# Performance work log

Measured on AMD Instinct MI355X. Metric: run time of the kernel, lower is better.

The kernel has to match this reference:

```python
import jax, jax.numpy as jnp
import numpy as np

B, M, N = 32, 2048, 2048
W_PRIMAL, W_DUAL, W_STAT, W_COMP = 0.1, 0.1, 0.6, 0.2


def setup_inputs() -> dict:
    key = jax.random.key(0)
    k1, k2, k3, k4, k5 = jax.random.split(key, 5)
    return {
        "x_hat": jax.random.normal(k1, (B * N,), dtype=jnp.float32),
        "lam_hat": jax.random.normal(k2, (B * M,), dtype=jnp.float32),
        "A": jax.random.normal(k3, (B, M, N), dtype=jnp.float32),
        "b_pad": jax.random.normal(k4, (B, M), dtype=jnp.float32),
        "c_pad": jax.random.normal(k5, (B, N), dtype=jnp.float32),
        "b_mask": jnp.ones((B, M), dtype=bool),
        "c_mask": jnp.ones((B, N), dtype=bool),
    }


def reference(x_hat, lam_hat, A, b_pad, c_pad, b_mask, c_mask):
    # Uniform sizes: x_hat is the concatenation of B vectors of length N,
    # lam_hat of B vectors of length M. b_mask/c_mask are unused by the
    # original forward (full padding assumed here).
    b, m, n = A.shape
    x = x_hat.reshape(b, n)
    lam = lam_hat.reshape(b, m)

    # Batched mat-vec products (the spmm calls in the original, fp32 math).
    Ax_minus_b = jnp.einsum("bmn,bn->bm", A, x) - b_pad        # [B, M]
    At_lambda = jnp.einsum("bmn,bm->bn", A, lam)               # [B, N]

    # Per-sample mean, summed over batch, then * (1/B) == global mean
    # (sizes are uniform).
    loss_primal = jnp.mean(jnp.square(jax.nn.relu(Ax_minus_b)))
    loss_dual = jnp.mean(jnp.square(jax.nn.relu(-lam)))
    loss_stat = jnp.mean(jnp.square(At_lambda + c_pad))
    loss_comp = jnp.mean(jnp.square(lam * Ax_minus_b))

    total = (W_PRIMAL * loss_primal + W_DUAL * loss_dual
             + W_STAT * loss_stat + W_COMP * loss_comp)
    return total
```

## Files before the change

### kernel.cpp

```cpp
#include <hip/hip_runtime.h>

#define BB 32
#define MM 2048
#define NN 2048
#define ROWS 64
#define THREADS 256


__device__ __forceinline__ float waveReduceSum(float v) {
#pragma unroll
    for (int off = 32; off > 0; off >>= 1)
        v += __shfl_down(v, off, 64);
    return v;
}

__global__ __launch_bounds__(256) void zero_ws_kernel(float* __restrict__ ws, int n) {
    int i = blockIdx.x * blockDim.x + threadIdx.x;
    if (i < n) ws[i] = 0.0f;
}

__global__ __launch_bounds__(THREADS) void fused_main(
    const float* __restrict__ x_hat, const float* __restrict__ lam_hat,
    const float* __restrict__ A, const float* __restrict__ b_pad,
    float* __restrict__ At, float* __restrict__ acc) {
    const int b = blockIdx.y;
    const int m0 = blockIdx.x * ROWS;
    const int t = threadIdx.x;
    const int wave = t >> 6;
    const int lane = t & 63;

    __shared__ float lamS[ROWS];
    __shared__ float wp[ROWS * 4];

    if (t < ROWS) lamS[t] = lam_hat[b * MM + m0 + t];
    __syncthreads();

    const float4* xv = (const float4*)(x_hat + (size_t)b * NN);
    const float4 x0 = xv[t];
    const float4 x1 = xv[256 + t];

    float4 at0 = make_float4(0.f, 0.f, 0.f, 0.f);
    float4 at1 = make_float4(0.f, 0.f, 0.f, 0.f);

    const float4* Ab = (const float4*)(A + ((size_t)b * MM + (size_t)m0) * NN);

    for (int r = 0; r < ROWS; ++r) {
        const float4* ap = Ab + (size_t)r * (NN / 4);
        float4 a0 = ap[t];
        float4 a1 = ap[256 + t];
        float lm = lamS[r];
        float dot = a0.x * x0.x + a0.y * x0.y + a0.z * x0.z + a0.w * x0.w
                  + a1.x * x1.x + a1.y * x1.y + a1.z * x1.z + a1.w * x1.w;
        at0.x += a0.x * lm; at0.y += a0.y * lm; at0.z += a0.z * lm; at0.w += a0.w * lm;
        at1.x += a1.x * lm; at1.y += a1.y * lm; at1.z += a1.z * lm; at1.w += a1.w * lm;
        float wsum = waveReduceSum(dot);
        if (lane == 0) wp[r * 4 + wave] = wsum;
    }
    __syncthreads();

    if (t < ROWS) {
        int r = t;
        float y = wp[r * 4 + 0] + wp[r * 4 + 1] + wp[r * 4 + 2] + wp[r * 4 + 3]
                - b_pad[b * MM + m0 + r];
        float lm = lamS[r];
        float ry = fmaxf(y, 0.f);
        float pr = ry * ry;
        float cm = lm * y;
        cm = cm * cm;
        pr = waveReduceSum(pr);
        cm = waveReduceSum(cm);
        if (t == 0) {
            atomicAdd(&acc[0], pr);
            atomicAdd(&acc[1], cm);
        }
    }

    float* Atb = At + (size_t)b * NN;
    int c0 = t * 4;
    atomicAdd(&Atb[c0 + 0], at0.x);
    atomicAdd(&Atb[c0 + 1], at0.y);
    atomicAdd(&Atb[c0 + 2], at0.z);
    atomicAdd(&Atb[c0 + 3], at0.w);
    atomicAdd(&Atb[1024 + c0 + 0], at1.x);
    atomicAdd(&Atb[1024 + c0 + 1], at1.y);
    atomicAdd(&Atb[1024 + c0 + 2], at1.z);
    atomicAdd(&Atb[1024 + c0 + 3], at1.w);
}

__global__ __launch_bounds__(256) void finalize_partial(
    const float* __restrict__ At, const float* __restrict__ c_pad,
    const float* __restrict__ lam_hat, float* __restrict__ acc) {
    int idx = blockIdx.x * blockDim.x + threadIdx.x;
    int stride = gridDim.x * blockDim.x;
    float stat = 0.f, dual = 0.f;
    for (int i = idx; i < BB * NN; i += stride) {
        float v = At[i] + c_pad[i];
        stat += v * v;
        float l = lam_hat[i];
        float rn = fmaxf(-l, 0.f);
        dual += rn * rn;
    }
    stat = waveReduceSum(stat);
    dual = waveReduceSum(dual);
    __shared__ float s[8];
    int wave = threadIdx.x >> 6, lane = threadIdx.x & 63;
    if (lane == 0) { s[wave * 2 + 0] = stat; s[wave * 2 + 1] = dual; }
    __syncthreads();
    if (threadIdx.x == 0) {
        atomicAdd(&acc[2], s[0] + s[2] + s[4] + s[6]);
        atomicAdd(&acc[3], s[1] + s[3] + s[5] + s[7]);
    }
}

__global__ void combine_kernel(const float* __restrict__ acc, float* __restrict__ out) {
    const float invBM = 1.0f / (float)(BB * MM);
    const float invBN = 1.0f / (float)(BB * NN);
    float primal = acc[0] * invBM;
    float comp   = acc[1] * invBM;
    float stat   = acc[2] * invBN;
    float dual   = acc[3] * invBM;
    out[0] = 0.1f * primal + 0.1f * dual + 0.6f * stat + 0.2f * comp;
}

extern "C" void kernel_launch(void* const* d_in, const int* in_sizes, int n_in,
                              void* d_out, int out_size, void* d_ws, size_t ws_size,
                              hipStream_t stream) {
    const float* x_hat   = (const float*)d_in[0];
    const float* lam_hat = (const float*)d_in[1];
    const float* A       = (const float*)d_in[2];
    const float* b_pad   = (const float*)d_in[3];
    const float* c_pad   = (const float*)d_in[4];
    float* out = (float*)d_out;

    float* At  = (float*)d_ws;
    float* acc = At + (size_t)BB * NN;

    const int ws_elems = BB * NN + 4;
    zero_ws_kernel<<<(ws_elems + 255) / 256, 256, 0, stream>>>((float*)d_ws, ws_elems);

    dim3 grid(MM / ROWS, BB);
    fused_main<<<grid, THREADS, 0, stream>>>(x_hat, lam_hat, A, b_pad, At, acc);

    finalize_partial<<<64, 256, 0, stream>>>(At, c_pad, lam_hat, acc);

    combine_kernel<<<1, 1, 0, stream>>>(acc, out);
}
```

Baseline: 711.5 us.

## Replace global atomics with per-chunk partial buffers and use nontemporal loads of A

Each main-kernel block now writes its A^T·lambda slice and its primal/complementarity partial sums to its own workspace slot instead of issuing atomicAdds into shared accumulators. The finalize kernel sums the 32 chunk partials per column, and a 256-thread combine kernel reduces the per-block results. This removes the zeroing kernel and atomic contention, and it makes the reduction deterministic. Loads of A use nontemporal hints so the large streaming matrix bypasses cache retention. The cost is an extra 8 MB partial buffer that is written and then re-read by a finalize kernel with only 64 blocks.

```diff
diff --git a/kernel.cpp b/kernel.cpp
--- a/kernel.cpp
+++ b/kernel.cpp
@@ -4,8 +4,14 @@
 #define MM 2048
 #define NN 2048
 #define ROWS 64
+#define CHUNKS (MM / ROWS)
 #define THREADS 256
 
+typedef float f32x4 __attribute__((ext_vector_type(4)));
+
+#define P0 ((size_t)BB * CHUNKS * NN)
+#define P1 (P0 + 2 * BB * CHUNKS)
+#define FIN_BLOCKS 64
 
 __device__ __forceinline__ float waveReduceSum(float v) {
 #pragma unroll
@@ -14,17 +20,13 @@
     return v;
 }
 
-__global__ __launch_bounds__(256) void zero_ws_kernel(float* __restrict__ ws, int n) {
-    int i = blockIdx.x * blockDim.x + threadIdx.x;
-    if (i < n) ws[i] = 0.0f;
-}
-
 __global__ __launch_bounds__(THREADS) void fused_main(
     const float* __restrict__ x_hat, const float* __restrict__ lam_hat,
     const float* __restrict__ A, const float* __restrict__ b_pad,
-    float* __restrict__ At, float* __restrict__ acc) {
+    float* __restrict__ ws) {
     const int b = blockIdx.y;
-    const int m0 = blockIdx.x * ROWS;
+    const int chunk = blockIdx.x;
+    const int m0 = chunk * ROWS;
     const int t = threadIdx.x;
     const int wave = t >> 6;
     const int lane = t & 63;
@@ -35,24 +37,24 @@
     if (t < ROWS) lamS[t] = lam_hat[b * MM + m0 + t];
     __syncthreads();
 
-    const float4* xv = (const float4*)(x_hat + (size_t)b * NN);
-    const float4 x0 = xv[t];
-    const float4 x1 = xv[256 + t];
+    const f32x4* xv = (const f32x4*)(x_hat + (size_t)b * NN);
+    const f32x4 x0 = xv[t];
+    const f32x4 x1 = xv[256 + t];
 
-    float4 at0 = make_float4(0.f, 0.f, 0.f, 0.f);
-    float4 at1 = make_float4(0.f, 0.f, 0.f, 0.f);
+    f32x4 at0 = (f32x4)(0.f);
+    f32x4 at1 = (f32x4)(0.f);
 
-    const float4* Ab = (const float4*)(A + ((size_t)b * MM + (size_t)m0) * NN);
+    const f32x4* Ab = (const f32x4*)(A + ((size_t)b * MM + (size_t)m0) * NN);
 
     for (int r = 0; r < ROWS; ++r) {
-        const float4* ap = Ab + (size_t)r * (NN / 4);
-        float4 a0 = ap[t];
-        float4 a1 = ap[256 + t];
+        const f32x4* ap = Ab + (size_t)r * (NN / 4);
+        f32x4 a0 = __builtin_nontemporal_load(ap + t);
+        f32x4 a1 = __builtin_nontemporal_load(ap + 256 + t);
         float lm = lamS[r];
-        float dot = a0.x * x0.x + a0.y * x0.y + a0.z * x0.z + a0.w * x0.w
-                  + a1.x * x1.x + a1.y * x1.y + a1.z * x1.z + a1.w * x1.w;
-        at0.x += a0.x * lm; at0.y += a0.y * lm; at0.z += a0.z * lm; at0.w += a0.w * lm;
-        at1.x += a1.x * lm; at1.y += a1.y * lm; at1.z += a1.z * lm; at1.w += a1.w * lm;
+        f32x4 d = a0 * x0 + a1 * x1;
+        float dot = d.x + d.y + d.z + d.w;
+        at0 += a0 * lm;
+        at1 += a1 * lm;
         float wsum = waveReduceSum(dot);
         if (lane == 0) wp[r * 4 + wave] = wsum;
     }
@@ -70,56 +72,76 @@
         pr = waveReduceSum(pr);
         cm = waveReduceSum(cm);
         if (t == 0) {
-            atomicAdd(&acc[0], pr);
-            atomicAdd(&acc[1], cm);
+            float* prcm = ws + P0 + ((size_t)b * CHUNKS + chunk) * 2;
+            prcm[0] = pr;
+            prcm[1] = cm;
         }
     }
 
-    float* Atb = At + (size_t)b * NN;
-    int c0 = t * 4;
-    atomicAdd(&Atb[c0 + 0], at0.x);
-    atomicAdd(&Atb[c0 + 1], at0.y);
-    atomicAdd(&Atb[c0 + 2], at0.z);
-    atomicAdd(&Atb[c0 + 3], at0.w);
-    atomicAdd(&Atb[1024 + c0 + 0], at1.x);
-    atomicAdd(&Atb[1024 + c0 + 1], at1.y);
-    atomicAdd(&Atb[1024 + c0 + 2], at1.z);
-    atomicAdd(&Atb[1024 + c0 + 3], at1.w);
+    f32x4* dst = (f32x4*)(ws + ((size_t)b * CHUNKS + chunk) * NN);
+    dst[t] = at0;
+    dst[256 + t] = at1;
 }
 
 __global__ __launch_bounds__(256) void finalize_partial(
-    const float* __restrict__ At, const float* __restrict__ c_pad,
-    const float* __restrict__ lam_hat, float* __restrict__ acc) {
+    const float* __restrict__ ws_ro, const float* __restrict__ c_pad,
+    const float* __restrict__ lam_hat, float* __restrict__ ws) {
     int idx = blockIdx.x * blockDim.x + threadIdx.x;
     int stride = gridDim.x * blockDim.x;
-    float stat = 0.f, dual = 0.f;
+    float stat = 0.f, dual = 0.f, pr = 0.f, cm = 0.f;
     for (int i = idx; i < BB * NN; i += stride) {
-        float v = At[i] + c_pad[i];
+        int b = i >> 11;
+        int col = i & (NN - 1);
+        const float* p = ws_ro + (size_t)b * CHUNKS * NN + col;
+        float s = 0.f;
+#pragma unroll
+        for (int k = 0; k < CHUNKS; ++k) s += p[(size_t)k * NN];
+        float v = s + c_pad[i];
         stat += v * v;
         float l = lam_hat[i];
         float rn = fmaxf(-l, 0.f);
         dual += rn * rn;
     }
+    for (int i = idx; i < BB * CHUNKS; i += stride) {
+        pr += ws_ro[P0 + 2 * i];
+        cm += ws_ro[P0 + 2 * i + 1];
+    }
     stat = waveReduceSum(stat);
     dual = waveReduceSum(dual);
-    __shared__ float s[8];
+    pr = waveReduceSum(pr);
+    cm = waveReduceSum(cm);
+    __shared__ float s[16];
     int wave = threadIdx.x >> 6, lane = threadIdx.x & 63;
-    if (lane == 0) { s[wave * 2 + 0] = stat; s[wave * 2 + 1] = dual; }
+    if (lane == 0) {
+        s[wave * 4 + 0] = stat; s[wave * 4 + 1] = dual;
+        s[wave * 4 + 2] = pr;   s[wave * 4 + 3] = cm;
+    }
     __syncthreads();
-    if (threadIdx.x == 0) {
-        atomicAdd(&acc[2], s[0] + s[2] + s[4] + s[6]);
-        atomicAdd(&acc[3], s[1] + s[3] + s[5] + s[7]);
+    if (threadIdx.x < 4) {
+        float v = s[threadIdx.x] + s[4 + threadIdx.x] + s[8 + threadIdx.x] + s[12 + threadIdx.x];
+        ws[P1 + (size_t)blockIdx.x * 4 + threadIdx.x] = v;
     }
 }
 
-__global__ void combine_kernel(const float* __restrict__ acc, float* __restrict__ out) {
-    const float invBM = 1.0f / (float)(BB * MM);
-    const float invBN = 1.0f / (float)(BB * NN);
-    float primal = acc[0] * invBM;
-    float comp   = acc[1] * invBM;
-    float stat   = acc[2] * invBN;
-    float dual   = acc[3] * invBM;
-    out[0] = 0.1f * primal + 0.1f * dual + 0.6f * stat + 0.2f * comp;
+__global__ __launch_bounds__(256) void combine_kernel(
+    const float* __restrict__ ws_ro, float* __restrict__ out) {
+    const int t = threadIdx.x;
+    const int wave = t >> 6;
+    const int lane = t & 63;
+    float v = ws_ro[P1 + (size_t)lane * 4 + wave];
+    v = waveReduceSum(v);
+    __shared__ float s[4];
+    if (lane == 0) s[wave] = v;
+    __syncthreads();
+    if (t == 0) {
+        const float invBM = 1.0f / (float)(BB * MM);
+        const float invBN = 1.0f / (float)(BB * NN);
+        float stat = s[0] * invBN;
+        float dual = s[1] * invBM;
+        float primal = s[2] * invBM;
+        float comp = s[3] * invBM;
+        out[0] = 0.1f * primal + 0.1f * dual + 0.6f * stat + 0.2f * comp;
+    }
 }
 
 extern "C" void kernel_launch(void* const* d_in, const int* in_sizes, int n_in,
@@ -131,17 +153,12 @@
     const float* b_pad   = (const float*)d_in[3];
     const float* c_pad   = (const float*)d_in[4];
     float* out = (float*)d_out;
+    float* ws = (float*)d_ws;
 
-    float* At  = (float*)d_ws;
-    float* acc = At + (size_t)BB * NN;
+    dim3 grid(CHUNKS, BB);
+    fused_main<<<grid, THREADS, 0, stream>>>(x_hat, lam_hat, A, b_pad, ws);
 
-    const int ws_elems = BB * NN + 4;
-    zero_ws_kernel<<<(ws_elems + 255) / 256, 256, 0, stream>>>((float*)d_ws, ws_elems);
+    finalize_partial<<<FIN_BLOCKS, 256, 0, stream>>>(ws, c_pad, lam_hat, ws);
 
-    dim3 grid(MM / ROWS, BB);
-    fused_main<<<grid, THREADS, 0, stream>>>(x_hat, lam_hat, A, b_pad, At, acc);
-
-    finalize_partial<<<64, 256, 0, stream>>>(At, c_pad, lam_hat, acc);
-
-    combine_kernel<<<1, 1, 0, stream>>>(acc, out);
+    combine_kernel<<<1, 256, 0, stream>>>(ws, out);
 }
```

Measured after the change: 664.0 us. -6.7%, faster.
